# Kernel tuning notes

Hardware: AMD Instinct MI355X
Metric: run time of the kernel (lower is better)

Reference implementation:

```python
import jax, jax.numpy as jnp
import numpy as np

NUM_HEADS = 8


def _conv3x3(x, w, b):
    # x: (B, C, H, W); w: (O, I, 3, 3) -> (B, O, H, W), stride 1, SAME padding
    y = jax.lax.conv_general_dilated(
        x, w, window_strides=(1, 1), padding='SAME',
        dimension_numbers=('NCHW', 'OIHW', 'NCHW'))
    return y + b[None, :, None, None]


def setup_inputs() -> dict:
    key = jax.random.key(0)
    ks = jax.random.split(key, 7)
    bs, mc, C, H, W = 2, 5, 640, 32, 32
    s = 0.02  # init scale for weights
    return {
        'x': jax.random.normal(ks[0], (bs, mc, C, H, W), jnp.float32),
        'wq': jax.random.normal(ks[1], (C, C, 3, 3), jnp.float32) * s,
        'bq': jnp.zeros((C,), jnp.float32),
        'wk': jax.random.normal(ks[2], (C, C, 3, 3), jnp.float32) * s,
        'bk': jnp.zeros((C,), jnp.float32),
        'wv': jax.random.normal(ks[3], (C, C, 3, 3), jnp.float32) * s,
        'bv': jnp.zeros((C,), jnp.float32),
        'w_proj': jax.random.normal(ks[4], (C, C), jnp.float32) * s,
        'b_proj': jnp.zeros((C,), jnp.float32),
    }


def reference(x, wq, bq, wk, bk, wv, bv, w_proj, b_proj):
    bs, mc, C, H, W = x.shape
    N = H * W
    nh = NUM_HEADS
    hd = C // nh
    scale = hd ** -0.5

    xf = x.reshape(bs * mc, C, H, W)

    def proj(w, b):
        # conv -> (bs, mc, nh, hd, N) -> (bs, mc, nh, N, hd)
        y = _conv3x3(xf, w, b).reshape(bs, mc, nh, hd, N)
        return y.transpose(0, 1, 2, 4, 3)

    q = proj(wq, bq)
    k = proj(wk, bk)
    v = proj(wv, bv)

    attn = jax.nn.softmax(jnp.einsum('bmhnd,bmhkd->bmhnk', q, k) * scale, axis=-1)
    o = jnp.einsum('bmhnk,bmhkd->bmhnd', attn, v)  # (bs, mc, nh, N, hd)

    # permute(0,3,1,2,4).reshape(bs, N, mc*C) then split back to (bs, N, mc, C)
    o = o.transpose(0, 3, 1, 2, 4).reshape(bs, N, mc, C)
    o = jnp.einsum('bnmc,dc->bnmd', o, w_proj) + b_proj  # Linear(C, C)
    return o.reshape(bs, N, mc * C)
```

## Files before the change

### kernel.cpp

```cpp
#include <hip/hip_runtime.h>

typedef _Float16 half_t;
typedef _Float16 half8 __attribute__((ext_vector_type(8)));
typedef _Float16 half4 __attribute__((ext_vector_type(4)));
typedef float floatx4 __attribute__((ext_vector_type(4)));
typedef unsigned int u32;

#define MFMA32(a,b,c) __builtin_amdgcn_mfma_f32_16x16x32_f16(a,b,c,0,0,0)
#define MFMA16(a,b,c) __builtin_amdgcn_mfma_f32_16x16x16f16(a,b,c,0,0,0)

#define XPAD_ELEMS (10u*34*34*640)
#define WR_ELEMS   (3u*9*640*640)
#define WP_ELEMS   (640u*640)
#define QKV_ELEMS  (10u*8*1024*80)
#define O_ELEMS    (10u*1024*640)

__device__ __forceinline__ void load16_lds(half_t* lds, const half_t* g) {
  __builtin_amdgcn_global_load_lds((const __attribute__((address_space(1))) u32*)g,
                                   (__attribute__((address_space(3))) u32*)lds,
                                   16, 0, 0);
}

__global__ __launch_bounds__(256) void k_convert_x(const float* __restrict__ x,
                                                   half_t* __restrict__ xpad) {
  const int img = blockIdx.x >> 5, y = blockIdx.x & 31;
  const float* src = x + (size_t)img*640*1024 + y*32;
  half_t* dst = xpad + (size_t)img*34*34*640;
  for (int i = threadIdx.x; i < 640*32; i += 256) {
    int xx = i / 640, c = i - xx*640;
    float v = src[(size_t)c*1024 + xx];
    dst[((size_t)(y+1)*34 + xx + 1)*640 + c] = (half_t)v;
  }
}

__global__ __launch_bounds__(256) void k_convert_w(const float* __restrict__ wq,
                                                   const float* __restrict__ wk,
                                                   const float* __restrict__ wv,
                                                   const float* __restrict__ wp,
                                                   half_t* __restrict__ wr2,
                                                   half_t* __restrict__ wp16) {
  __shared__ half_t tr[9*644];
  const int p = blockIdx.y, row = blockIdx.x;
  if (p < 3) {
    const float* W = (p == 0) ? wq : (p == 1) ? wk : wv;
    const float* src = W + (size_t)row*5760;
    for (int j = threadIdx.x; j < 5760; j += 256) {
      int ci = j / 9, t = j - ci*9;
      tr[t*644 + ci] = (half_t)src[j];
    }
    __syncthreads();
    half_t* dst = wr2 + ((size_t)p*640 + row)*5760;
    for (int i = threadIdx.x; i < 5760; i += 256) {
      int t = i / 640, ci = i - t*640;
      dst[i] = tr[t*644 + ci];
    }
  } else {
    for (int i = threadIdx.x; i < 640; i += 256)
      wp16[(size_t)row*640 + i] = (half_t)wp[(size_t)row*640 + i];
  }
}

#define TRC(T) (((T)/3)*34 + ((T) - ((T)/3)*3))
#define K0C(T) ((((T)+2)%9)*640 + (((T)+2)/9)*32)

__global__ __launch_bounds__(512) void k_conv(const half_t* __restrict__ xpad,
                                              const half_t* __restrict__ wr2,
                                              const float* __restrict__ bq,
                                              const float* __restrict__ bk,
                                              const float* __restrict__ bv,
                                              half_t* __restrict__ qo,
                                              half_t* __restrict__ ko,
                                              half_t* __restrict__ vo) {
  __shared__ __align__(16) half_t sX[2][1536*8];
  __shared__ __align__(16) half_t sW[3][640*8];
  const int tid = threadIdx.x;
  const int lane = tid & 63, wv = tid >> 6;
  const int l15 = lane & 15, lq = lane >> 4, lq16 = lq*16;
  const int id = blockIdx.x;
  const int wg = (id >> 3) + (id & 7)*60;
  const int mt = wg & 3;
  const int rest = wg >> 2;
  const int nt = rest & 3;
  const int z  = rest >> 2;
  const int proj = z / 10, img = z - proj*10;

  const half_t* xg  = xpad + ((size_t)img*34*34 + (size_t)mt*8*34)*640;
  const half_t* wgp = wr2 + ((size_t)proj*640 + nt*160)*5760;

  int xsrc[3];
#pragma unroll
  for (int kk = 0; kk < 3; ++kk) {
    int unit = kk*512 + tid;
    int row = unit >> 2, sub = unit & 3;
    int ch = sub ^ ((row >> 1) & 3);
    xsrc[kk] = row*640 + ch*8;
  }
  int wsrc0, wsrc1;
  { int row = tid >> 2, sub = tid & 3;
    int ch = sub ^ ((row >> 1) & 3);
    wsrc0 = row*5760 + ch*8; }
  { int unit = 512 + tid;
    int row = unit >> 2, sub = unit & 3;
    int ch = sub ^ ((row >> 1) & 3);
    wsrc1 = row*5760 + ch*8; }

  const int wm = wv >> 1, wn = wv & 1;
  int arow0[4];
#pragma unroll
  for (int fr = 0; fr < 4; ++fr) {
    int p = wm*64 + fr*16 + l15;
    arow0[fr] = (p >> 5)*34 + (p & 31);
  }
  int bbase;
  { int r = wn*80 + l15;
    bbase = r*64 + (lq16 ^ (((r >> 1) & 3) << 4)); }

#pragma unroll
  for (int kk = 0; kk < 3; ++kk)
    load16_lds(sX[0] + (size_t)(kk*512 + wv*64)*8, xg + xsrc[kk]);
  load16_lds(sW[0] + (size_t)(wv*64)*8, wgp + wsrc0);
  if (wv < 2) load16_lds(sW[0] + (size_t)(512 + wv*64)*8, wgp + wsrc1);
  load16_lds(sW[1] + (size_t)(wv*64)*8, wgp + wsrc0 + 640);
  if (wv < 2) load16_lds(sW[1] + (size_t)(512 + wv*64)*8, wgp + wsrc1 + 640);
  if (wv < 2) asm volatile("s_waitcnt vmcnt(2)" ::: "memory");
  else        asm volatile("s_waitcnt vmcnt(1)" ::: "memory");
  asm volatile("s_barrier" ::: "memory");

  floatx4 acc[4][5] = {};

#define STEP_BODY(T, SXR, DOW, K0E, DOX, VMN)                                      \
  do {                                                                             \
    half8 Av[4], Aw0, Aw1;                                                         \
    { const char* sXc = (const char*)(SXR);                                        \
      const char* sWc = (const char*)(sW[(T)%3]);                                  \
      _Pragma("unroll")                                                            \
      for (int fr = 0; fr < 4; ++fr) {                                             \
        int r = arow0[fr] + TRC(T);                                                \
        Av[fr] = *(const half8*)(sXc + r*64 + (lq16 ^ (((r>>1)&3)<<4)));           \
      }                                                                            \
      Aw0 = *(const half8*)(sWc + bbase);                                          \
      Aw1 = *(const half8*)(sWc + bbase + 1024); }                                 \
    if (DOW) {                                                                     \
      load16_lds(sW[((T)+2)%3] + (size_t)(wv*64)*8, wgp + wsrc0 + (K0E));          \
      if (wv < 2)                                                                  \
        load16_lds(sW[((T)+2)%3] + (size_t)(512 + wv*64)*8, wgp + wsrc1 + (K0E));  \
    }                                                                              \
    if (DOX) {                                                                     \
      _Pragma("unroll")                                                            \
      for (int kk = 0; kk < 3; ++kk)                                               \
        load16_lds(sxw + (size_t)(kk*512 + wv*64)*8, xg + xsrc[kk] + (g+1)*32);    \
    }                                                                              \
    if ((VMN) == 2) {                                                              \
      if (wv < 2) asm volatile("s_waitcnt vmcnt(5)" ::: "memory");                 \
      else        asm volatile("s_waitcnt vmcnt(4)" ::: "memory");                 \
    } else if ((VMN) == 1) {                                                       \
      if (wv < 2) asm volatile("s_waitcnt vmcnt(2)" ::: "memory");                 \
      else        asm volatile("s_waitcnt vmcnt(1)" ::: "memory");                 \
    } else {                                                                       \
      asm volatile("s_waitcnt vmcnt(0)" ::: "memory");                             \
    }                                                                              \
    asm volatile("s_barrier" ::: "memory");                                        \
    __builtin_amdgcn_sched_barrier(0);                                             \
    __builtin_amdgcn_s_setprio(1);                                                 \
    { const char* sWc = (const char*)(sW[(T)%3]);                                  \
      half8 Aw2 = *(const half8*)(sWc + bbase + 2048);                             \
      _Pragma("unroll")                                                            \
      for (int fr = 0; fr < 4; ++fr) acc[fr][0] = MFMA32(Av[fr], Aw0, acc[fr][0]); \
      half8 Aw3 = *(const half8*)(sWc + bbase + 3072);                             \
      _Pragma("unroll")                                                            \
      for (int fr = 0; fr < 4; ++fr) acc[fr][1] = MFMA32(Av[fr], Aw1, acc[fr][1]); \
      half8 Aw4 = *(const half8*)(sWc + bbase + 4096);                             \
      _Pragma("unroll")                                                            \
      for (int fr = 0; fr < 4; ++fr) acc[fr][2] = MFMA32(Av[fr], Aw2, acc[fr][2]); \
      _Pragma("unroll")                                                            \
      for (int fr = 0; fr < 4; ++fr) acc[fr][3] = MFMA32(Av[fr], Aw3, acc[fr][3]); \
      _Pragma("unroll")                                                            \
      for (int fr = 0; fr < 4; ++fr) acc[fr][4] = MFMA32(Av[fr], Aw4, acc[fr][4]); \
    }                                                                              \
    __builtin_amdgcn_s_setprio(0);                                                 \
    asm volatile("s_barrier" ::: "memory");                                        \
  } while (0)

  for (int g = 0; g < 19; ++g) {
    half_t* sxr = sX[g & 1];
    half_t* sxw = sX[(g + 1) & 1];
    STEP_BODY(0, sxr, 1, K0C(0) + g*32, 0, 1);
    STEP_BODY(1, sxr, 1, K0C(1) + g*32, 0, 1);
    STEP_BODY(2, sxr, 1, K0C(2) + g*32, 0, 1);
    STEP_BODY(3, sxr, 1, K0C(3) + g*32, 0, 1);
    STEP_BODY(4, sxr, 1, K0C(4) + g*32, 0, 1);
    STEP_BODY(5, sxr, 1, K0C(5) + g*32, 1, 2);
    STEP_BODY(6, sxr, 1, K0C(6) + g*32, 0, 1);
    STEP_BODY(7, sxr, 1, K0C(7) + g*32, 0, 1);
    STEP_BODY(8, sxr, 1, K0C(8) + g*32, 0, 1);
  }
  {
    const int g = 19;
    half_t* sxr = sX[1];
    half_t* sxw = sX[0];
    (void)sxw;
    STEP_BODY(0, sxr, 1, K0C(0) + 19*32, 0, 1);
    STEP_BODY(1, sxr, 1, K0C(1) + 19*32, 0, 1);
    STEP_BODY(2, sxr, 1, K0C(2) + 19*32, 0, 1);
    STEP_BODY(3, sxr, 1, K0C(3) + 19*32, 0, 1);
    STEP_BODY(4, sxr, 1, K0C(4) + 19*32, 0, 1);
    STEP_BODY(5, sxr, 1, K0C(5) + 19*32, 0, 1);
    STEP_BODY(6, sxr, 1, K0C(6) + 19*32, 0, 1);
    STEP_BODY(7, sxr, 0, 0, 0, 0);
    STEP_BODY(8, sxr, 0, 0, 0, 0);
    (void)g;
  }
#undef STEP_BODY

  const float* bias = (proj == 0) ? bq : (proj == 1) ? bk : bv;
#pragma unroll
  for (int fc = 0; fc < 5; ++fc) {
    int co = nt*160 + wn*80 + fc*16 + l15;
    float bb = bias[co];
    int hh = 2*nt + wn;
    int d  = fc*16 + l15;
#pragma unroll
    for (int fr = 0; fr < 4; ++fr)
#pragma unroll
      for (int j = 0; j < 4; ++j) {
        int n = mt*256 + wm*64 + fr*16 + lq*4 + j;
        float val = acc[fr][fc][j] + bb;
        if (proj == 0)      qo[((size_t)(img*8 + hh)*1024 + n)*80 + d] = (half_t)(val * 0.11180339887498949f);
        else if (proj == 1) ko[((size_t)(img*8 + hh)*1024 + n)*80 + d] = (half_t)val;
        else                vo[((size_t)(img*8 + hh)*80 + d)*1024 + n] = (half_t)val;
      }
  }
}

__global__ __launch_bounds__(256) void k_attn(const half_t* __restrict__ qg_,
                                              const half_t* __restrict__ kg_,
                                              const half_t* __restrict__ vg_,
                                              half_t* __restrict__ og_) {
  __shared__ __align__(16) half_t sQ[128*80];
  __shared__ __align__(16) half_t sK[2][64*80];
  __shared__ __align__(16) half_t sV[2][80*64];
  __shared__ __align__(16) half_t sP[128*64];
  const int tid = threadIdx.x, lane = tid & 63, wv = tid >> 6;
  const int l15 = lane & 15, lq = lane >> 4;
  const int id = blockIdx.x;
  const int wgb = (id >> 3) + (id & 7)*80;
  const int qt = wgb & 7, gh = wgb >> 3;
  const half_t* qg = qg_ + ((size_t)gh*1024 + qt*128)*80;
  const half_t* kg = kg_ + (size_t)gh*1024*80;
  const half_t* vg = vg_ + (size_t)gh*80*1024;

#define STAGE_KV(kt, buf) do {                                                \
    _Pragma("unroll")                                                         \
    for (int kk = 0; kk < 3; ++kk) {                                          \
      int c = kk*256 + tid;                                                   \
      if (c < 640) {                                                          \
        int row = c / 10, cw = c - row*10;                                    \
        load16_lds(sK[buf] + (size_t)(kk*256 + wv*64)*8,                      \
                   kg + ((size_t)(kt)*64 + row)*80 + cw*8);                   \
      }                                                                       \
    }                                                                         \
    _Pragma("unroll")                                                         \
    for (int kk = 0; kk < 3; ++kk) {                                          \
      int c = kk*256 + tid;                                                   \
      if (c < 640) {                                                          \
        load16_lds(sV[buf] + (size_t)(kk*256 + wv*64)*8,                      \
                   vg + (size_t)(c >> 3)*1024 + (kt)*64 + (c & 7)*8);         \
      }                                                                       \
    }                                                                         \
  } while (0)

#pragma unroll
  for (int kk = 0; kk < 5; ++kk)
    load16_lds(sQ + (size_t)(kk*256 + wv*64)*8, qg + (size_t)(kk*256 + tid)*8);
  STAGE_KV(0, 0);
  asm volatile("s_waitcnt vmcnt(0)" ::: "memory");
  __builtin_amdgcn_s_barrier();
  __builtin_amdgcn_sched_barrier(0);

  half8 qa0[2], qa1[2]; half4 qa2[2];
  {
    const char* sQb = (const char*)sQ;
#pragma unroll
    for (int fr = 0; fr < 2; ++fr) {
      int r = wv*32 + fr*16 + l15;
      qa0[fr] = *(const half8*)(sQb + r*160 + lq*16);
      qa1[fr] = *(const half8*)(sQb + r*160 + 64 + lq*16);
      qa2[fr] = *(const half4*)(sQb + r*160 + 128 + lq*8);
    }
  }

  float mrow[2][4], lrow[2][4];
  floatx4 oacc[2][5] = {};
#pragma unroll
  for (int fr = 0; fr < 2; ++fr)
#pragma unroll
    for (int j = 0; j < 4; ++j) { mrow[fr][j] = -1e30f; lrow[fr][j] = 0.f; }

  for (int kt = 0; kt < 16; ++kt) {
    const int cur = kt & 1;
    if (kt < 15) STAGE_KV(kt + 1, cur ^ 1);

    const char* sKb = (const char*)sK[cur];
    floatx4 s[2][4];
#pragma unroll
    for (int fc = 0; fc < 4; ++fc) {
      int key = fc*16 + l15;
      half8 kb0 = *(const half8*)(sKb + key*160 + lq*16);
      half8 kb1 = *(const half8*)(sKb + key*160 + 64 + lq*16);
      half4 kb2 = *(const half4*)(sKb + key*160 + 128 + lq*8);
#pragma unroll
      for (int fr = 0; fr < 2; ++fr) {
        floatx4 t = {0.f, 0.f, 0.f, 0.f};
        t = MFMA16(qa2[fr], kb2, t);
        t = MFMA32(qa0[fr], kb0, t);
        t = MFMA32(qa1[fr], kb1, t);
        s[fr][fc] = t;
      }
    }

    float corr[2][4], psum[2][4];
#pragma unroll
    for (int fr = 0; fr < 2; ++fr)
#pragma unroll
      for (int j = 0; j < 4; ++j) {
        float mx = fmaxf(fmaxf(s[fr][0][j], s[fr][1][j]), fmaxf(s[fr][2][j], s[fr][3][j]));
        mx = fmaxf(mx, __shfl_xor(mx, 1));
        mx = fmaxf(mx, __shfl_xor(mx, 2));
        mx = fmaxf(mx, __shfl_xor(mx, 4));
        mx = fmaxf(mx, __shfl_xor(mx, 8));
        float mn = fmaxf(mrow[fr][j], mx);
        corr[fr][j] = __expf(mrow[fr][j] - mn);
        mrow[fr][j] = mn;
        psum[fr][j] = 0.f;
      }
#pragma unroll
    for (int fc = 0; fc < 4; ++fc)
#pragma unroll
      for (int fr = 0; fr < 2; ++fr)
#pragma unroll
        for (int j = 0; j < 4; ++j) {
          float p = __expf(s[fr][fc][j] - mrow[fr][j]);
          psum[fr][j] += p;
          sP[(size_t)(wv*32 + fr*16 + lq*4 + j)*64 + fc*16 + l15] = (half_t)p;
        }
#pragma unroll
    for (int fr = 0; fr < 2; ++fr)
#pragma unroll
      for (int j = 0; j < 4; ++j) {
        float t2 = psum[fr][j];
        t2 += __shfl_xor(t2, 1);
        t2 += __shfl_xor(t2, 2);
        t2 += __shfl_xor(t2, 4);
        t2 += __shfl_xor(t2, 8);
        lrow[fr][j] = lrow[fr][j]*corr[fr][j] + t2;
      }
#pragma unroll
    for (int fr = 0; fr < 2; ++fr)
#pragma unroll
      for (int fc = 0; fc < 5; ++fc)
#pragma unroll
        for (int j = 0; j < 4; ++j)
          oacc[fr][fc][j] *= corr[fr][j];

    asm volatile("s_waitcnt lgkmcnt(0)" ::: "memory");
    __builtin_amdgcn_s_barrier();
    __builtin_amdgcn_sched_barrier(0);

    const char* sPb = (const char*)sP;
    const char* sVb = (const char*)sV[cur];
    half8 pa[2][2];
#pragma unroll
    for (int fr = 0; fr < 2; ++fr) {
      int r = wv*32 + fr*16 + l15;
#pragma unroll
      for (int ks = 0; ks < 2; ++ks)
        pa[fr][ks] = *(const half8*)(sPb + r*128 + ks*64 + lq*16);
    }
#pragma unroll
    for (int fc = 0; fc < 5; ++fc)
#pragma unroll
      for (int ks = 0; ks < 2; ++ks) {
        half8 vb = *(const half8*)(sVb + (fc*16 + l15)*128 + ks*64 + lq*16);
#pragma unroll
        for (int fr = 0; fr < 2; ++fr)
          oacc[fr][fc] = MFMA32(pa[fr][ks], vb, oacc[fr][fc]);
      }

    asm volatile("s_waitcnt vmcnt(0) lgkmcnt(0)" ::: "memory");
    __builtin_amdgcn_s_barrier();
    __builtin_amdgcn_sched_barrier(0);
  }
#undef STAGE_KV

  const int img = gh >> 3, hh = gh & 7;
  half_t* og = og_ + ((size_t)img*1024 + qt*128)*640 + hh*80;
#pragma unroll
  for (int fr = 0; fr < 2; ++fr)
#pragma unroll
    for (int j = 0; j < 4; ++j) {
      int n = wv*32 + fr*16 + lq*4 + j;
      float inv = 1.f / lrow[fr][j];
#pragma unroll
      for (int fc = 0; fc < 5; ++fc)
        og[(size_t)n*640 + fc*16 + l15] = (half_t)(oacc[fr][fc][j] * inv);
    }
}

__global__ __launch_bounds__(256) void k_proj(const half_t* __restrict__ oa,
                                              const half_t* __restrict__ wp,
                                              const float* __restrict__ bp,
                                              float* __restrict__ out) {
  __shared__ __align__(16) half_t sA[128*32];
  __shared__ __align__(16) half_t sB[128*32];
  const int tid = threadIdx.x, lane = tid & 63, wv = tid >> 6;
  const int l15 = lane & 15, lq = lane >> 4;
  const int mt = blockIdx.x, nt = blockIdx.y, img = blockIdx.z;
  const int bb = img / 5, mm = img - bb*5;
  const half_t* ag = oa + ((size_t)img*1024 + mt*128)*640;
  const half_t* bg = wp + (size_t)nt*128*640;
  const int wrow = (wv >> 1)*64, wcol = (wv & 1)*64;
  floatx4 acc[4][4] = {};
  for (int g = 0; g < 20; ++g) {
    __syncthreads();
#pragma unroll
    for (int kk = 0; kk < 2; ++kk) {
      int c = kk*256 + tid;
      load16_lds(sA + (size_t)(kk*256 + wv*64)*8, ag + (size_t)(c >> 2)*640 + g*32 + (c & 3)*8);
      load16_lds(sB + (size_t)(kk*256 + wv*64)*8, bg + (size_t)(c >> 2)*640 + g*32 + (c & 3)*8);
    }
    __syncthreads();
    const char* sAb = (const char*)sA;
    const char* sBb = (const char*)sB;
    half8 av[4], bw[4];
#pragma unroll
    for (int fr = 0; fr < 4; ++fr) av[fr] = *(const half8*)(sAb + (wrow + fr*16 + l15)*64 + lq*16);
#pragma unroll
    for (int fc = 0; fc < 4; ++fc) bw[fc] = *(const half8*)(sBb + (wcol + fc*16 + l15)*64 + lq*16);
#pragma unroll
    for (int fr = 0; fr < 4; ++fr)
#pragma unroll
      for (int fc = 0; fc < 4; ++fc)
        acc[fr][fc] = MFMA32(av[fr], bw[fc], acc[fr][fc]);
  }
  float* og = out + ((size_t)bb*1024 + mt*128)*3200 + mm*640 + nt*128;
#pragma unroll
  for (int fc = 0; fc < 4; ++fc) {
    float bias = bp[nt*128 + wcol + fc*16 + l15];
#pragma unroll
    for (int fr = 0; fr < 4; ++fr)
#pragma unroll
      for (int j = 0; j < 4; ++j)
        og[(size_t)(wrow + fr*16 + lq*4 + j)*3200 + wcol + fc*16 + l15] = acc[fr][fc][j] + bias;
  }
}

extern "C" void kernel_launch(void* const* d_in, const int* in_sizes, int n_in,
                              void* d_out, int out_size, void* d_ws, size_t ws_size,
                              hipStream_t stream) {
  const float* x  = (const float*)d_in[0];
  const float* wq = (const float*)d_in[1];
  const float* bq = (const float*)d_in[2];
  const float* wk = (const float*)d_in[3];
  const float* bk = (const float*)d_in[4];
  const float* wv = (const float*)d_in[5];
  const float* bv = (const float*)d_in[6];
  const float* wp = (const float*)d_in[7];
  const float* bp = (const float*)d_in[8];
  float* out = (float*)d_out;

  half_t* xpad = (half_t*)d_ws;
  half_t* wr2  = xpad + XPAD_ELEMS;
  half_t* wp16 = wr2 + WR_ELEMS;
  half_t* q    = wp16 + WP_ELEMS;
  half_t* k    = q + QKV_ELEMS;
  half_t* v    = k + QKV_ELEMS;
  half_t* oa   = v + QKV_ELEMS;

  (void)hipMemsetAsync(xpad, 0, (size_t)XPAD_ELEMS*sizeof(half_t), stream);
  k_convert_x<<<320, 256, 0, stream>>>(x, xpad);
  k_convert_w<<<dim3(640, 4), 256, 0, stream>>>(wq, wk, wv, wp, wr2, wp16);
  k_conv<<<480, 512, 0, stream>>>(xpad, wr2, bq, bk, bv, q, k, v);
  k_attn<<<640, 256, 0, stream>>>(q, k, v, oa);
  k_proj<<<dim3(8, 5, 10), 256, 0, stream>>>(oa, wp16, bp, out);
}
```

Before: 413.9 us.

## Drop trailing barrier per conv step and interleave A-fragment LDS reads with MFMAs

Reworks the implicit-GEMM conv inner step so all five weight fragments and one activation fragment are read before the barrier. The other three activation fragments are read interleaved with the MFMA chain. The second barrier per step is removed, relying on the triple-buffered weight ring and an explicit lgkmcnt(0) wait before the barrier. The X prefetch moves from step 5 to step 6, with an adjusted vmcnt at step 7. This halves barrier count but risks LDS write-after-read races on the double-buffered X tile and register pressure from holding more fragments.

```diff
diff --git a/kernel.cpp b/kernel.cpp
--- a/kernel.cpp
+++ b/kernel.cpp
@@ -128,18 +128,18 @@
 
   floatx4 acc[4][5] = {};
 
-#define STEP_BODY(T, SXR, DOW, K0E, DOX, VMN)                                      \
+#define STEP1(T, DOW, K0E, DOX, VMW)                                               \
   do {                                                                             \
-    half8 Av[4], Aw0, Aw1;                                                         \
-    { const char* sXc = (const char*)(SXR);                                        \
+    half8 Av0, Aw0, Aw1, Aw2, Aw3, Aw4;                                            \
+    { const char* sXc = (const char*)sxr;                                          \
       const char* sWc = (const char*)(sW[(T)%3]);                                  \
-      _Pragma("unroll")                                                            \
-      for (int fr = 0; fr < 4; ++fr) {                                             \
-        int r = arow0[fr] + TRC(T);                                                \
-        Av[fr] = *(const half8*)(sXc + r*64 + (lq16 ^ (((r>>1)&3)<<4)));           \
-      }                                                                            \
+      int r0 = arow0[0] + TRC(T);                                                  \
+      Av0 = *(const half8*)(sXc + r0*64 + (lq16 ^ (((r0>>1)&3)<<4)));              \
       Aw0 = *(const half8*)(sWc + bbase);                                          \
-      Aw1 = *(const half8*)(sWc + bbase + 1024); }                                 \
+      Aw1 = *(const half8*)(sWc + bbase + 1024);                                   \
+      Aw2 = *(const half8*)(sWc + bbase + 2048);                                   \
+      Aw3 = *(const half8*)(sWc + bbase + 3072);                                   \
+      Aw4 = *(const half8*)(sWc + bbase + 4096); }                                 \
     if (DOW) {                                                                     \
       load16_lds(sW[((T)+2)%3] + (size_t)(wv*64)*8, wgp + wsrc0 + (K0E));          \
       if (wv < 2)                                                                  \
@@ -150,67 +150,80 @@
       for (int kk = 0; kk < 3; ++kk)                                               \
         load16_lds(sxw + (size_t)(kk*512 + wv*64)*8, xg + xsrc[kk] + (g+1)*32);    \
     }                                                                              \
-    if ((VMN) == 2) {                                                              \
+    if ((VMW) == 2) {                                                              \
       if (wv < 2) asm volatile("s_waitcnt vmcnt(5)" ::: "memory");                 \
       else        asm volatile("s_waitcnt vmcnt(4)" ::: "memory");                 \
-    } else if ((VMN) == 1) {                                                       \
+    } else if ((VMW) == 1) {                                                       \
       if (wv < 2) asm volatile("s_waitcnt vmcnt(2)" ::: "memory");                 \
       else        asm volatile("s_waitcnt vmcnt(1)" ::: "memory");                 \
     } else {                                                                       \
       asm volatile("s_waitcnt vmcnt(0)" ::: "memory");                             \
     }                                                                              \
+    asm volatile("s_waitcnt lgkmcnt(0)" ::: "memory");                             \
     asm volatile("s_barrier" ::: "memory");                                        \
     __builtin_amdgcn_sched_barrier(0);                                             \
     __builtin_amdgcn_s_setprio(1);                                                 \
-    { const char* sWc = (const char*)(sW[(T)%3]);                                  \
-      half8 Aw2 = *(const half8*)(sWc + bbase + 2048);                             \
-      _Pragma("unroll")                                                            \
-      for (int fr = 0; fr < 4; ++fr) acc[fr][0] = MFMA32(Av[fr], Aw0, acc[fr][0]); \
-      half8 Aw3 = *(const half8*)(sWc + bbase + 3072);                             \
-      _Pragma("unroll")                                                            \
-      for (int fr = 0; fr < 4; ++fr) acc[fr][1] = MFMA32(Av[fr], Aw1, acc[fr][1]); \
-      half8 Aw4 = *(const half8*)(sWc + bbase + 4096);                             \
-      _Pragma("unroll")                                                            \
-      for (int fr = 0; fr < 4; ++fr) acc[fr][2] = MFMA32(Av[fr], Aw2, acc[fr][2]); \
-      _Pragma("unroll")                                                            \
-      for (int fr = 0; fr < 4; ++fr) acc[fr][3] = MFMA32(Av[fr], Aw3, acc[fr][3]); \
-      _Pragma("unroll")                                                            \
-      for (int fr = 0; fr < 4; ++fr) acc[fr][4] = MFMA32(Av[fr], Aw4, acc[fr][4]); \
+    { const char* sXc = (const char*)sxr;                                          \
+      int r1 = arow0[1] + TRC(T);                                                  \
+      half8 Av1 = *(const half8*)(sXc + r1*64 + (lq16 ^ (((r1>>1)&3)<<4)));        \
+      acc[0][0] = MFMA32(Av0, Aw0, acc[0][0]);                                     \
+      acc[0][1] = MFMA32(Av0, Aw1, acc[0][1]);                                     \
+      acc[0][2] = MFMA32(Av0, Aw2, acc[0][2]);                                     \
+      int r2 = arow0[2] + TRC(T);                                                  \
+      half8 Av2 = *(const half8*)(sXc + r2*64 + (lq16 ^ (((r2>>1)&3)<<4)));        \
+      acc[0][3] = MFMA32(Av0, Aw3, acc[0][3]);                                     \
+      acc[0][4] = MFMA32(Av0, Aw4, acc[0][4]);                                     \
+      int r3 = arow0[3] + TRC(T);                                                  \
+      half8 Av3 = *(const half8*)(sXc + r3*64 + (lq16 ^ (((r3>>1)&3)<<4)));        \
+      acc[1][0] = MFMA32(Av1, Aw0, acc[1][0]);                                     \
+      acc[1][1] = MFMA32(Av1, Aw1, acc[1][1]);                                     \
+      acc[1][2] = MFMA32(Av1, Aw2, acc[1][2]);                                     \
+      acc[1][3] = MFMA32(Av1, Aw3, acc[1][3]);                                     \
+      acc[1][4] = MFMA32(Av1, Aw4, acc[1][4]);                                     \
+      acc[2][0] = MFMA32(Av2, Aw0, acc[2][0]);                                     \
+      acc[2][1] = MFMA32(Av2, Aw1, acc[2][1]);                                     \
+      acc[2][2] = MFMA32(Av2, Aw2, acc[2][2]);                                     \
+      acc[2][3] = MFMA32(Av2, Aw3, acc[2][3]);                                     \
+      acc[2][4] = MFMA32(Av2, Aw4, acc[2][4]);                                     \
+      acc[3][0] = MFMA32(Av3, Aw0, acc[3][0]);                                     \
+      acc[3][1] = MFMA32(Av3, Aw1, acc[3][1]);                                     \
+      acc[3][2] = MFMA32(Av3, Aw2, acc[3][2]);                                     \
+      acc[3][3] = MFMA32(Av3, Aw3, acc[3][3]);                                     \
+      acc[3][4] = MFMA32(Av3, Aw4, acc[3][4]);                                     \
     }                                                                              \
     __builtin_amdgcn_s_setprio(0);                                                 \
-    asm volatile("s_barrier" ::: "memory");                                        \
   } while (0)
 
   for (int g = 0; g < 19; ++g) {
     half_t* sxr = sX[g & 1];
     half_t* sxw = sX[(g + 1) & 1];
-    STEP_BODY(0, sxr, 1, K0C(0) + g*32, 0, 1);
-    STEP_BODY(1, sxr, 1, K0C(1) + g*32, 0, 1);
-    STEP_BODY(2, sxr, 1, K0C(2) + g*32, 0, 1);
-    STEP_BODY(3, sxr, 1, K0C(3) + g*32, 0, 1);
-    STEP_BODY(4, sxr, 1, K0C(4) + g*32, 0, 1);
-    STEP_BODY(5, sxr, 1, K0C(5) + g*32, 1, 2);
-    STEP_BODY(6, sxr, 1, K0C(6) + g*32, 0, 1);
-    STEP_BODY(7, sxr, 1, K0C(7) + g*32, 0, 1);
-    STEP_BODY(8, sxr, 1, K0C(8) + g*32, 0, 1);
+    STEP1(0, 1, K0C(0) + g*32, 0, 1);
+    STEP1(1, 1, K0C(1) + g*32, 0, 1);
+    STEP1(2, 1, K0C(2) + g*32, 0, 1);
+    STEP1(3, 1, K0C(3) + g*32, 0, 1);
+    STEP1(4, 1, K0C(4) + g*32, 0, 1);
+    STEP1(5, 1, K0C(5) + g*32, 0, 1);
+    STEP1(6, 1, K0C(6) + g*32, 1, 2);
+    STEP1(7, 1, K0C(7) + g*32, 0, 2);
+    STEP1(8, 1, K0C(8) + g*32, 0, 1);
   }
   {
     const int g = 19;
     half_t* sxr = sX[1];
     half_t* sxw = sX[0];
     (void)sxw;
-    STEP_BODY(0, sxr, 1, K0C(0) + 19*32, 0, 1);
-    STEP_BODY(1, sxr, 1, K0C(1) + 19*32, 0, 1);
-    STEP_BODY(2, sxr, 1, K0C(2) + 19*32, 0, 1);
-    STEP_BODY(3, sxr, 1, K0C(3) + 19*32, 0, 1);
-    STEP_BODY(4, sxr, 1, K0C(4) + 19*32, 0, 1);
-    STEP_BODY(5, sxr, 1, K0C(5) + 19*32, 0, 1);
-    STEP_BODY(6, sxr, 1, K0C(6) + 19*32, 0, 1);
-    STEP_BODY(7, sxr, 0, 0, 0, 0);
-    STEP_BODY(8, sxr, 0, 0, 0, 0);
+    STEP1(0, 1, K0C(0) + 19*32, 0, 1);
+    STEP1(1, 1, K0C(1) + 19*32, 0, 1);
+    STEP1(2, 1, K0C(2) + 19*32, 0, 1);
+    STEP1(3, 1, K0C(3) + 19*32, 0, 1);
+    STEP1(4, 1, K0C(4) + 19*32, 0, 1);
+    STEP1(5, 1, K0C(5) + 19*32, 0, 1);
+    STEP1(6, 1, K0C(6) + 19*32, 0, 1);
+    STEP1(7, 0, 0, 0, 0);
+    STEP1(8, 0, 0, 0, 0);
     (void)g;
   }
-#undef STEP_BODY
+#undef STEP1
 
   const float* bias = (proj == 0) ? bq : (proj == 1) ? bk : bv;
 #pragma unroll
```

Measured after the change: 398.2 us. 3.8% less time.
